# Kernel tuning notes

Hardware: AMD Instinct MI355X
Metric: run time of the kernel (lower is better)

The kernel has to match this reference:

```python
import jax, jax.numpy as jnp
import numpy as np

HEADS = 4


def _forward(x_atoms, pos, edge_attr, molecular_features, emb_W, emb_b, mp_W1, mp_b1, mp_W2, mp_b2, ln_g, ln_b, attn_in_w, attn_in_b, attn_out_w, attn_out_b, pool_W, pool_b, mol_gate, lrn_gate, molemb_W1, molemb_b1, molemb_W2, molemb_b2, lrnemb_W1, lrnemb_b1, lrnemb_W2, lrnemb_b2, fus_W1, fus_b1, fus_W2, fus_b2, head_W1, head_b1, head_W2, head_b2, edge_index, batch_idx):
    N = x_atoms.shape[0]
    B = molecular_features.shape[0]
    A = N // B  # equal-size molecules; batch_idx = repeat(arange(B), A)
    H = emb_W.shape[1]
    L = mp_W1.shape[0]
    src, dst = edge_index[0], edge_index[1]  # PyG: x_j = x[src], x_i = x[dst]
    x = x_atoms @ emb_W + emb_b
    # distance features (constant across layers)
    diff = pos[dst] - pos[src]
    d = jnp.sqrt(jnp.sum(diff * diff, axis=1, keepdims=True) + 1e-12)
    dist_feat = jnp.concatenate([d, 1.0 / (1.0 + d), jnp.exp(-d)], axis=1)  # [E,3]
    ones_e = jnp.ones((src.shape[0], 1), x.dtype)
    cnt = jnp.maximum(jax.ops.segment_sum(ones_e, dst, num_segments=N), 1.0)
    for l in range(L):
        res = x
        msg = jnp.concatenate([x[dst], x[src], dist_feat], axis=1)  # [E, 2H+3]
        msg = jax.nn.relu(msg @ mp_W1[l] + mp_b1[l]) @ mp_W2[l] + mp_b2[l]
        x = jax.ops.segment_sum(msg, dst, num_segments=N) / cnt  # mean aggregation
        y = x + res
        mu = y.mean(-1, keepdims=True)
        var = jnp.var(y, axis=-1, keepdims=True)
        x = (y - mu) * jax.lax.rsqrt(var + 1e-5) * ln_g[l] + ln_b[l]
    xm = x.reshape(B, A, H)
    explicit = xm.mean(axis=1)  # scatter_mean over equal-size graphs
    # per-molecule multi-head self-attention (torch MHA, eval mode)
    hd = H // HEADS
    qkv = xm @ attn_in_w.T + attn_in_b
    q, k, v = jnp.split(qkv, 3, axis=-1)
    q = q.reshape(B, A, HEADS, hd)
    k = k.reshape(B, A, HEADS, hd)
    v = v.reshape(B, A, HEADS, hd)
    scores = jnp.einsum('bqhd,bkhd->bhqk', q, k) / jnp.sqrt(jnp.asarray(hd, x.dtype))
    att = jax.nn.softmax(scores, axis=-1)
    o = jnp.einsum('bhqk,bkhd->bqhd', att, v).reshape(B, A, H)
    attended = o @ attn_out_w.T + attn_out_b
    aw = jax.nn.softmax(jnp.sum(attended * xm, axis=-1), axis=1)  # [B,A]
    wmean = jnp.sum(attended * aw[..., None], axis=1)
    maxp = attended.max(axis=1)
    meanp = attended.mean(axis=1)
    stdp = jnp.std(attended, axis=1, ddof=1)  # torch.std unbiased
    pooled = jnp.stack([wmean, maxp, meanp, stdp], axis=0)  # [4,B,H]
    proj = jnp.einsum('kbh,khf->kbf', pooled, pool_W) + pool_b[:, None, :]
    learned = jnp.moveaxis(proj, 0, 1).reshape(B, -1)  # [B,LF]
    # per-property gated MLPs, vectorized over P (atom gates are computed but unused in the source)
    gm = molecular_features[None] * jax.nn.sigmoid(mol_gate)[:, None, :]
    gl = learned[None] * jax.nn.sigmoid(lrn_gate)[:, None, :]
    molrep = jax.nn.relu(jnp.einsum('pbm,pmh->pbh', gm, molemb_W1) + molemb_b1[:, None, :])
    molrep = jnp.einsum('pbh,phk->pbk', molrep, molemb_W2) + molemb_b2[:, None, :]
    lrnrep = jax.nn.relu(jnp.einsum('pbm,pmh->pbh', gl, lrnemb_W1) + lrnemb_b1[:, None, :])
    lrnrep = jnp.einsum('pbh,phk->pbk', lrnrep, lrnemb_W2) + lrnemb_b2[:, None, :]
    P = mol_gate.shape[0]
    comb = jnp.concatenate([jnp.broadcast_to(explicit[None], (P, B, H)), molrep, lrnrep], axis=-1)
    fused = jax.nn.relu(jnp.einsum('pbc,pch->pbh', comb, fus_W1) + fus_b1[:, None, :])
    fused = jnp.einsum('pbh,phk->pbk', fused, fus_W2) + fus_b2[:, None, :]
    h = jax.nn.relu(jnp.einsum('pbh,phk->pbk', fused, head_W1) + head_b1[:, None, :])
    out = jnp.einsum('pbk,pko->pbo', h, head_W2) + head_b2[:, None, :]
    return out  # [P,B,1]: stacked predictions for the 4 properties


def setup_inputs() -> dict:
    key = jax.random.key(0)
    ks = jax.random.split(key, 24)
    B, A, F, M, H, LF, L, P = 1024, 32, 64, 200, 128, 64, 3, 4
    N = B * A
    E = N * 16
    H2, H4, Q = H // 2, H // 4, LF // 4
    n = lambda i, shape, s=1.0: jax.random.normal(ks[i], shape, dtype=jnp.float32) * s
    inp = {}
    inp['x_atoms'] = n(0, (N, F))
    inp['pos'] = n(1, (N, 3)) * 3.0
    inp['edge_attr'] = n(2, (E, 4))
    inp['molecular_features'] = n(3, (B, M))
    inp['emb_W'] = n(4, (F, H), 0.1)
    inp['emb_b'] = jnp.zeros((H,), jnp.float32)
    inp['mp_W1'] = n(5, (L, 2 * H + 3, H), 0.05)
    inp['mp_b1'] = jnp.zeros((L, H), jnp.float32)
    inp['mp_W2'] = n(6, (L, H, H), 0.05)
    inp['mp_b2'] = jnp.zeros((L, H), jnp.float32)
    inp['ln_g'] = jnp.ones((L, H), jnp.float32)
    inp['ln_b'] = jnp.zeros((L, H), jnp.float32)
    inp['attn_in_w'] = n(7, (3 * H, H), 0.08)
    inp['attn_in_b'] = jnp.zeros((3 * H,), jnp.float32)
    inp['attn_out_w'] = n(8, (H, H), 0.08)
    inp['attn_out_b'] = jnp.zeros((H,), jnp.float32)
    inp['pool_W'] = n(9, (4, H, Q), 0.08)
    inp['pool_b'] = jnp.zeros((4, Q), jnp.float32)
    inp['mol_gate'] = n(10, (P, M))
    inp['lrn_gate'] = n(11, (P, LF))
    inp['molemb_W1'] = n(12, (P, M, H2), 0.08)
    inp['molemb_b1'] = jnp.zeros((P, H2), jnp.float32)
    inp['molemb_W2'] = n(13, (P, H2, H2), 0.08)
    inp['molemb_b2'] = jnp.zeros((P, H2), jnp.float32)
    inp['lrnemb_W1'] = n(14, (P, LF, H2), 0.08)
    inp['lrnemb_b1'] = jnp.zeros((P, H2), jnp.float32)
    inp['lrnemb_W2'] = n(15, (P, H2, H2), 0.08)
    inp['lrnemb_b2'] = jnp.zeros((P, H2), jnp.float32)
    inp['fus_W1'] = n(16, (P, 2 * H, H), 0.08)
    inp['fus_b1'] = jnp.zeros((P, H), jnp.float32)
    inp['fus_W2'] = n(17, (P, H, H2), 0.08)
    inp['fus_b2'] = jnp.zeros((P, H2), jnp.float32)
    inp['head_W1'] = n(18, (P, H2, H4), 0.08)
    inp['head_b1'] = jnp.zeros((P, H4), jnp.float32)
    inp['head_W2'] = n(19, (P, H4, 1), 0.08)
    inp['head_b2'] = jnp.zeros((P, 1), jnp.float32)
    inp['edge_index'] = jax.random.randint(ks[20], (2, E), 0, N)
    inp['batch_idx'] = jnp.repeat(jnp.arange(B), A)
    return inp


def reference(x_atoms, pos, edge_attr, molecular_features, emb_W, emb_b, mp_W1, mp_b1, mp_W2, mp_b2, ln_g, ln_b, attn_in_w, attn_in_b, attn_out_w, attn_out_b, pool_W, pool_b, mol_gate, lrn_gate, molemb_W1, molemb_b1, molemb_W2, molemb_b2, lrnemb_W1, lrnemb_b1, lrnemb_W2, lrnemb_b2, fus_W1, fus_b1, fus_W2, fus_b2, head_W1, head_b1, head_W2, head_b2, edge_index, batch_idx):
    return _forward(x_atoms, pos, edge_attr, molecular_features, emb_W, emb_b, mp_W1, mp_b1, mp_W2, mp_b2, ln_g, ln_b, attn_in_w, attn_in_b, attn_out_w, attn_out_b, pool_W, pool_b, mol_gate, lrn_gate, molemb_W1, molemb_b1, molemb_W2, molemb_b2, lrnemb_W1, lrnemb_b1, lrnemb_W2, lrnemb_b2, fus_W1, fus_b1, fus_W2, fus_b2, head_W1, head_b1, head_W2, head_b2, edge_index, batch_idx)
```

## Files before the change

### kernel.cpp

```cpp
#include <hip/hip_runtime.h>

#define NE 524288
#define NN 32768
#define NB 1024

#define F4(p) (*(const float4*)(p))

typedef __bf16 bf16x8 __attribute__((ext_vector_type(8)));
typedef float  f32x4  __attribute__((ext_vector_type(4)));

__device__ __forceinline__ float sigmoidf_(float v) { return 1.f / (1.f + expf(-v)); }

__device__ __forceinline__ void bf16split(float f, short &hi, short &lo) {
  unsigned u = __float_as_uint(f);
  unsigned rh = (u + 0x7FFFu + ((u >> 16) & 1u)) >> 16;
  float fh = __uint_as_float(rh << 16);
  float fl = f - fh;
  unsigned u2 = __float_as_uint(fl);
  unsigned rl = (u2 + 0x7FFFu + ((u2 >> 16) & 1u)) >> 16;
  hi = (short)rh; lo = (short)rl;
}

__device__ __forceinline__ unsigned short f2bf(float f) {
  unsigned u = __float_as_uint(f);
// ... 19 lines not shown
    s = fmaf(xr[i],   ww.x, s);
    s = fmaf(xr[i+1], ww.y, s);
    s = fmaf(xr[i+2], ww.z, s);
    s = fmaf(xr[i+3], ww.w, s);
  }
  return s;
}

__global__ __launch_bounds__(128) void embed_kernel(
    const float* __restrict__ xa, const float* __restrict__ W,
    const float* __restrict__ b, float* __restrict__ x)
{
  __shared__ float a[64];
  const int n = blockIdx.x, t = threadIdx.x;
  if (t < 64) a[t] = xa[n*64 + t];
  __syncthreads();
  float s = b[t];
#pragma unroll 8
  for (int f = 0; f < 64; ++f) s = fmaf(a[f], W[f*128 + t], s);
  x[n*128 + t] = s;
}

__global__ __launch_bounds__(256) void hist_kernel(const int* __restrict__ ei, int* __restrict__ cnt) {
  const int e = blockIdx.x*256 + threadIdx.x;
  atomicAdd(&cnt[ei[NE + e]], 1);
}

__global__ __launch_bounds__(1024) void scan_kernel(
    const int* __restrict__ cnt, int* __restrict__ off, int* __restrict__ cur)
{
  __shared__ int wsum[16];
  const int t = threadIdx.x;
  int local[32];
  const int base = t*32;
  int s = 0;
#pragma unroll
  for (int i = 0; i < 32; ++i) { local[i] = cnt[base+i]; s += local[i]; }
  int pre = s;
  const int lane = t & 63;
#pragma unroll
  for (int o = 1; o < 64; o <<= 1) { int v = __shfl_up(pre, o); if (lane >= o) pre += v; }
  if (lane == 63) wsum[t >> 6] = pre;
  __syncthreads();
  if (t == 0) { int a = 0; for (int w = 0; w < 16; ++w) { int v = wsum[w]; wsum[w] = a; a += v; } }
  __syncthreads();
  int excl = wsum[t >> 6] + pre - s;
#pragma unroll
  for (int i = 0; i < 32; ++i) { off[base+i] = excl; cur[base+i] = excl; excl += local[i]; }
  if (t == 1023) off[NN] = excl;
}

__global__ __launch_bounds__(256) void scatter_kernel(
    const float* __restrict__ pos, const int* __restrict__ ei,
    int* __restrict__ cur, int* __restrict__ csr_src, float* __restrict__ csr_df)
{
  const int e = blockIdx.x*256 + threadIdx.x;
  const int s = ei[e];
  const int d = ei[NE + e];
  float dx = pos[d*3+0] - pos[s*3+0];
  float dy = pos[d*3+1] - pos[s*3+1];
  float dz = pos[d*3+2] - pos[s*3+2];
  float dist = sqrtf(dx*dx + dy*dy + dz*dz + 1e-12f);
  const int slot = atomicAdd(&cur[d], 1);
  csr_src[slot] = s;
  csr_df[slot*3+0] = dist;
  csr_df[slot*3+1] = 1.f/(1.f + dist);
  csr_df[slot*3+2] = expf(-dist);
}

__device__ __forceinline__ void pack_decode(int r, int N, int &k, int &n) {
  const int j = r & 7, lane = (r >> 3) & 63, rest = r >> 9;
  const int NT = N >> 4;
  const int t = rest % NT, kc = rest / NT;
  k = kc*32 + (lane >> 4)*8 + j;
  n = t*16 + (lane & 15);
}

__global__ __launch_bounds__(256) void prep_kernel(
    const float* __restrict__ mp_W1, const float* __restrict__ mp_W2,
    const float* __restrict__ win, const float* __restrict__ wout,
    const float* __restrict__ mp_b1,
    short* __restrict__ bh, short* __restrict__ bl, float* __restrict__ pqbias)
{
  const int i = blockIdx.x*256 + threadIdx.x;
  if (i < 768) { const int l = i >> 8, t = i & 255; pqbias[i] = t < 128 ? mp_b1[l*128 + t] : 0.f; }
  if (i >= 212992) return;
  int k, n; float v;
  if (i < 98304) {
    const int l = i / 32768, r = i % 32768;
    pack_decode(r, 256, k, n);
    const float* W = mp_W1 + (size_t)l*259*128;
    v = (n < 128) ? W[k*128 + n] : W[(128+k)*128 + (n-128)];
  } else if (i < 147456) {
    const int q = i - 98304, l = q / 16384, r = q % 16384;
    pack_decode(r, 128, k, n);
    v = mp_W2[(size_t)l*16384 + k*128 + n];
  } else if (i < 196608) {
    const int r = i - 147456;
    pack_decode(r, 384, k, n);
    v = win[n*128 + k];
  } else {
    const int r = i - 196608;
    pack_decode(r, 128, k, n);
    v = wout[n*128 + k];
  }
  short h, lo; bf16split(v, h, lo);
  bh[i] = h; bl[i] = lo;
}

__global__ __launch_bounds__(256, 2) void mfma_gemm_kernel(
    const float* __restrict__ A, int lda,
    const short* __restrict__ Bh, const short* __restrict__ Bl,
    const float* __restrict__ bias, float* __restrict__ C, int ncols, int ldc,
    unsigned short* __restrict__ qbf)
{
  const int lane = threadIdx.x & 63, wid = threadIdx.x >> 6;
  const int m0 = blockIdx.x * 128 + wid * 32;
  const int n0 = blockIdx.y * 64;
  const int NT = ncols >> 4;
  const int cl = lane & 15, kg = lane >> 4;

  bf16x8 Ah[2][4], Al[2][4];
#pragma unroll
  for (int s = 0; s < 2; ++s)
#pragma unroll
    for (int kc = 0; kc < 4; ++kc) {
      const float* ap = &A[(size_t)(m0 + s*16 + cl)*lda + kc*32 + kg*8];
      const float4 f0 = F4(ap), f1 = F4(ap + 4);
      const float fv[8] = {f0.x,f0.y,f0.z,f0.w,f1.x,f1.y,f1.z,f1.w};
      union { short s[8]; bf16x8 b; } uh, ul;
#pragma unroll
      for (int j = 0; j < 8; ++j) bf16split(fv[j], uh.s[j], ul.s[j]);
      Ah[s][kc] = uh.b; Al[s][kc] = ul.b;
    }

  f32x4 acc[2][4];
#pragma unroll
  for (int s = 0; s < 2; ++s)
#pragma unroll
    for (int t = 0; t < 4; ++t) acc[s][t] = (f32x4){0.f,0.f,0.f,0.f};

#pragma unroll
  for (int kc = 0; kc < 4; ++kc) {
    bf16x8 Bfh[4], Bfl[4];
#pragma unroll
    for (int t = 0; t < 4; ++t) {
      const size_t off = (((size_t)(kc*NT + (n0 >> 4) + t))*64 + lane)*8;
      Bfh[t] = *(const bf16x8*)&Bh[off];
      Bfl[t] = *(const bf16x8*)&Bl[off];
    }
#pragma unroll
    for (int s = 0; s < 2; ++s)
#pragma unroll
      for (int t = 0; t < 4; ++t)
        acc[s][t] = __builtin_amdgcn_mfma_f32_16x16x32_bf16(Ah[s][kc], Bfh[t], acc[s][t], 0, 0, 0);
#pragma unroll
    for (int s = 0; s < 2; ++s)
#pragma unroll
      for (int t = 0; t < 4; ++t)
        acc[s][t] = __builtin_amdgcn_mfma_f32_16x16x32_bf16(Ah[s][kc], Bfl[t], acc[s][t], 0, 0, 0);
#pragma unroll
    for (int s = 0; s < 2; ++s)
#pragma unroll
      for (int t = 0; t < 4; ++t)
        acc[s][t] = __builtin_amdgcn_mfma_f32_16x16x32_bf16(Al[s][kc], Bfh[t], acc[s][t], 0, 0, 0);
  }

#pragma unroll
  for (int t = 0; t < 4; ++t) {
    const int col = n0 + t*16 + cl;
    const float bv = bias[col];
#pragma unroll
    for (int s = 0; s < 2; ++s) {
      const int rbase = m0 + s*16 + kg*4;
#pragma unroll
      for (int r = 0; r < 4; ++r) {
        const float v = acc[s][t][r] + bv;
        if (qbf && col >= 128)
          qbf[(size_t)(rbase + r)*128 + (col - 128)] = f2bf(v);
        else
          C[(size_t)(rbase + r)*ldc + col] = v;
      }
    }
  }
}

__global__ __launch_bounds__(256, 2) void mfma_gemm_ln_kernel(
    const float* __restrict__ A, int lda,
    const short* __restrict__ Bh, const short* __restrict__ Bl,
    const float* __restrict__ b2, const int* __restrict__ csr_off,
    const float* __restrict__ g, const float* __restrict__ bb,
    float* __restrict__ x)
{
  const int lane = threadIdx.x & 63, wid = threadIdx.x >> 6;
  const int m0 = blockIdx.x * 64 + wid * 16;
  const int cl = lane & 15, kg = lane >> 4;

  bf16x8 Ah[4], Al[4];
#pragma unroll
  for (int kc = 0; kc < 4; ++kc) {
    const float* ap = &A[(size_t)(m0 + cl)*lda + kc*32 + kg*8];
    const float4 f0 = F4(ap), f1 = F4(ap + 4);
    const float fv[8] = {f0.x,f0.y,f0.z,f0.w,f1.x,f1.y,f1.z,f1.w};
    union { short s[8]; bf16x8 b; } uh, ul;
#pragma unroll
    for (int j = 0; j < 8; ++j) bf16split(fv[j], uh.s[j], ul.s[j]);
    Ah[kc] = uh.b; Al[kc] = ul.b;
  }

  f32x4 acc[8];
#pragma unroll
  for (int t = 0; t < 8; ++t) acc[t] = (f32x4){0.f,0.f,0.f,0.f};

#pragma unroll
  for (int kc = 0; kc < 4; ++kc) {
    bf16x8 Bfh[8], Bfl[8];
#pragma unroll
    for (int t = 0; t < 8; ++t) {
      const size_t off = (((size_t)(kc*8 + t))*64 + lane)*8;
      Bfh[t] = *(const bf16x8*)&Bh[off];
      Bfl[t] = *(const bf16x8*)&Bl[off];
    }
#pragma unroll
    for (int t = 0; t < 8; ++t)
      acc[t] = __builtin_amdgcn_mfma_f32_16x16x32_bf16(Ah[kc], Bfh[t], acc[t], 0, 0, 0);
#pragma unroll
    for (int t = 0; t < 8; ++t)
      acc[t] = __builtin_amdgcn_mfma_f32_16x16x32_bf16(Ah[kc], Bfl[t], acc[t], 0, 0, 0);
#pragma unroll
    for (int t = 0; t < 8; ++t)
      acc[t] = __builtin_amdgcn_mfma_f32_16x16x32_bf16(Al[kc], Bfh[t], acc[t], 0, 0, 0);
  }

  const int r0 = m0 + kg*4;
  float sflag[4];
#pragma unroll
  for (int r = 0; r < 4; ++r)
    sflag[r] = (csr_off[r0 + r + 1] > csr_off[r0 + r]) ? 1.f : 0.f;

  float ps[4] = {0.f,0.f,0.f,0.f}, pq[4] = {0.f,0.f,0.f,0.f};
  float yv[8][4];
#pragma unroll
  for (int t = 0; t < 8; ++t) {
    const int col = t*16 + cl;
    const float b2v = b2[col];
#pragma unroll
    for (int r = 0; r < 4; ++r) {
      const float y = acc[t][r] + sflag[r]*b2v + x[(size_t)(r0 + r)*128 + col];
      yv[t][r] = y;
      ps[r] += y;
      pq[r] = fmaf(y, y, pq[r]);
    }
  }
#pragma unroll
  for (int o = 1; o < 16; o <<= 1) {
#pragma unroll
    for (int r = 0; r < 4; ++r) { ps[r] += __shfl_xor(ps[r], o); pq[r] += __shfl_xor(pq[r], o); }
  }
#pragma unroll
  for (int r = 0; r < 4; ++r) {
    const float mu = ps[r] * (1.f/128.f);
    const float var = pq[r]*(1.f/128.f) - mu*mu;
    const float rstd = rsqrtf(var + 1e-5f);
#pragma unroll
    for (int t = 0; t < 8; ++t) {
      const int col = t*16 + cl;
      x[(size_t)(r0 + r)*128 + col] = (yv[t][r] - mu)*rstd*g[col] + bb[col];
    }
  }
}

__global__ __launch_bounds__(256, 6) void agg_kernel(
    float* __restrict__ P, const unsigned short* __restrict__ Qbf,
    const int* __restrict__ csr_off, const int* __restrict__ csr_src,
    const float* __restrict__ csr_df, const float* __restrict__ W1)
{
  const int tid = threadIdx.x;
  const int node = blockIdx.x*4 + (tid >> 6);
  const int lane = tid & 63;
  const int c0 = lane*2;
  const int off0 = csr_off[node], off1 = csr_off[node+1];

  const float* __restrict__ w1c = W1 + 256*128;
  const float w00 = w1c[c0],       w01 = w1c[c0+1];
  const float w10 = w1c[128+c0],   w11 = w1c[128+c0+1];
  const float w20 = w1c[256+c0],   w21 = w1c[256+c0+1];
  const float2 p = *(const float2*)&P[(size_t)node*128 + c0];

  float a0 = 0.f, a1 = 0.f;
  int e = off0;
  for (; e + 8 <= off1; e += 8) {
    int sr[8];
#pragma unroll
    for (int j = 0; j < 8; ++j) sr[j] = csr_src[e+j];
    ushort2 qv[8];
#pragma unroll
    for (int j = 0; j < 8; ++j) qv[j] = *(const ushort2*)&Qbf[(size_t)sr[j]*128 + c0];
    float dfv[8][3];
#pragma unroll
    for (int j = 0; j < 8; ++j) {
      dfv[j][0] = csr_df[(e+j)*3+0];
      dfv[j][1] = csr_df[(e+j)*3+1];
      dfv[j][2] = csr_df[(e+j)*3+2];
    }
#pragma unroll
    for (int j = 0; j < 8; ++j) {
      float h0 = p.x + bf2f(qv[j].x);
      h0 = fmaf(dfv[j][0], w00, h0); h0 = fmaf(dfv[j][1], w10, h0); h0 = fmaf(dfv[j][2], w20, h0);
      float h1 = p.y + bf2f(qv[j].y);
      h1 = fmaf(dfv[j][0], w01, h1); h1 = fmaf(dfv[j][1], w11, h1); h1 = fmaf(dfv[j][2], w21, h1);
      a0 += fmaxf(h0, 0.f);
      a1 += fmaxf(h1, 0.f);
    }
  }
  for (; e < off1; ++e) {
    const ushort2 qv = *(const ushort2*)&Qbf[(size_t)csr_src[e]*128 + c0];
    const float d0 = csr_df[e*3+0], d1 = csr_df[e*3+1], d2 = csr_df[e*3+2];
    float h0 = p.x + bf2f(qv.x);
    h0 = fmaf(d0, w00, h0); h0 = fmaf(d1, w10, h0); h0 = fmaf(d2, w20, h0);
    float h1 = p.y + bf2f(qv.y);
    h1 = fmaf(d0, w01, h1); h1 = fmaf(d1, w11, h1); h1 = fmaf(d2, w21, h1);
    a0 += fmaxf(h0, 0.f);
    a1 += fmaxf(h1, 0.f);
  }
  const int deg = off1 - off0;
  const float rc = deg > 0 ? 1.f/(float)deg : 1.f;
  *(float2*)&P[(size_t)node*128 + c0] = make_float2(a0*rc, a1*rc);
}

__global__ __launch_bounds__(128) void attn_kernel(float* __restrict__ dqkv)
{
  __shared__ float sk[32*132];
  __shared__ float sv[32*132];
  const int tid = threadIdx.x;
  const int b = blockIdx.x;

  for (int idx = tid; idx < 1024; idx += 128) {
    const int a = idx >> 5, c4 = idx & 31;
    *(float4*)&sk[a*132 + c4*4] = F4(&dqkv[(size_t)(b*32+a)*384 + 128 + c4*4]);
    *(float4*)&sv[a*132 + c4*4] = F4(&dqkv[(size_t)(b*32+a)*384 + 256 + c4*4]);
  }
  __syncthreads();

  const int h = tid >> 5, qr = tid & 31;
  float qreg[32];
  ld32(qreg, &dqkv[(size_t)(b*32+qr)*384 + h*32]);

  float sc[32];
#pragma unroll
  for (int k = 0; k < 32; ++k)
    sc[k] = dot32r(&sk[k*132 + h*32], qreg) * 0.17677669529663687f;
  float mx = sc[0];
#pragma unroll
  for (int k = 1; k < 32; ++k) mx = fmaxf(mx, sc[k]);
  float se = 0.f;
#pragma unroll
  for (int k = 0; k < 32; ++k) { sc[k] = expf(sc[k] - mx); se += sc[k]; }
  const float inv = 1.f / se;

  __syncthreads();

  float od[32];
#pragma unroll
  for (int i = 0; i < 32; ++i) od[i] = 0.f;
#pragma unroll 4
  for (int k = 0; k < 32; ++k) {
    const float w = sc[k] * inv;
    const float* vr = &sv[k*132 + h*32];
#pragma unroll
    for (int i = 0; i < 32; i += 4) {
      float4 v = F4(&vr[i]);
      od[i]   = fmaf(w, v.x, od[i]);
      od[i+1] = fmaf(w, v.y, od[i+1]);
      od[i+2] = fmaf(w, v.z, od[i+2]);
      od[i+3] = fmaf(w, v.w, od[i+3]);
    }
  }
#pragma unroll
  for (int i = 0; i < 32; i += 4)
    *(float4*)&sk[qr*132 + h*32 + i] = make_float4(od[i], od[i+1], od[i+2], od[i+3]);
  __syncthreads();

  for (int idx = tid; idx < 1024; idx += 128) {
    const int a = idx >> 5, c4 = idx & 31;
    *(float4*)&dqkv[(size_t)(b*32+a)*384 + 256 + c4*4] = F4(&sk[a*132 + c4*4]);
  }
}

__global__ __launch_bounds__(128) void pool_kernel(
    const float* __restrict__ att, const float* __restrict__ x,
    const float* __restrict__ pW, const float* __restrict__ pb,
    float* __restrict__ expl, float* __restrict__ lrn)
{
  __shared__ float satt[32*132];
  __shared__ float sx[32*132];
  __shared__ float aw_l[32];
  __shared__ float spool[512];
  const int tid = threadIdx.x;
  const int b = blockIdx.x;

  for (int idx = tid; idx < 1024; idx += 128) {
    const int a = idx >> 5, c4 = idx & 31;
    *(float4*)&satt[a*132 + c4*4] = F4(&att[(size_t)(b*32+a)*128 + c4*4]);
    *(float4*)&sx[a*132 + c4*4]   = F4(&x[(size_t)(b*32+a)*128 + c4*4]);
  }
  __syncthreads();

  {
    const int a = tid >> 2, q4 = tid & 3;
    float sp = 0.f;
#pragma unroll
    for (int i = 0; i < 32; ++i)
      sp = fmaf(satt[a*132 + q4*32 + i], sx[a*132 + q4*32 + i], sp);
    sp += __shfl_xor(sp, 1);
    sp += __shfl_xor(sp, 2);
    if (q4 == 0) aw_l[a] = sp;
  }
  __syncthreads();

  {
    float awr[32];
    float mxl = aw_l[0];
#pragma unroll
    for (int a = 1; a < 32; ++a) mxl = fmaxf(mxl, aw_l[a]);
    float se = 0.f;
#pragma unroll
    for (int a = 0; a < 32; ++a) { awr[a] = expf(aw_l[a] - mxl); se += awr[a]; }
    const float inv = 1.f / se;
    const int c = tid;
    float mx = -3.4e38f, sm = 0.f, wm = 0.f, ex = 0.f;
#pragma unroll
    for (int a = 0; a < 32; ++a) {
      const float v = satt[a*132 + c];
      mx = fmaxf(mx, v);
      sm += v;
      wm = fmaf(v, awr[a], wm);
      ex += sx[a*132 + c];
    }
    wm *= inv;
    const float mean = sm * 0.03125f;
    float s2 = 0.f;
#pragma unroll
    for (int a = 0; a < 32; ++a) {
      const float d = satt[a*132 + c] - mean;
      s2 = fmaf(d, d, s2);
    }
    const float stdp = sqrtf(s2 * (1.f/31.f));
    expl[b*128 + c] = ex * 0.03125f;
    spool[c]       = wm;
    spool[128 + c] = mx;
    spool[256 + c] = mean;
    spool[384 + c] = stdp;
  }
  __syncthreads();

  if (tid < 64) {
    const int k = tid >> 4, qq = tid & 15;
    const float* pk = pW + k*2048;
    float s0 = 0.f, s1 = 0.f, s2 = 0.f, s3 = 0.f;
    for (int h2 = 0; h2 < 128; h2 += 4) {
      s0 = fmaf(spool[k*128 + h2],   pk[h2*16 + qq],     s0);
      s1 = fmaf(spool[k*128 + h2+1], pk[(h2+1)*16 + qq], s1);
      s2 = fmaf(spool[k*128 + h2+2], pk[(h2+2)*16 + qq], s2);
      s3 = fmaf(spool[k*128 + h2+3], pk[(h2+3)*16 + qq], s3);
    }
    lrn[b*64 + tid] = pb[k*16 + qq] + (s0+s1) + (s2+s3);
  }
}

__global__ __launch_bounds__(64) void head_kernel(
    const float* __restrict__ molf, const float* __restrict__ lrn,
    const float* __restrict__ expl,
    const float* __restrict__ mol_gate, const float* __restrict__ lrn_gate,
    const float* __restrict__ meW1, const float* __restrict__ meb1,
    const float* __restrict__ meW2, const float* __restrict__ meb2,
    const float* __restrict__ leW1, const float* __restrict__ leb1,
    const float* __restrict__ leW2, const float* __restrict__ leb2,
    const float* __restrict__ fW1, const float* __restrict__ fb1,
    const float* __restrict__ fW2, const float* __restrict__ fb2,
    const float* __restrict__ hW1, const float* __restrict__ hb1,
    const float* __restrict__ hW2, const float* __restrict__ hb2,
    float* __restrict__ out)
{
  const int b = blockIdx.x, p = blockIdx.y, t = threadIdx.x;
  __shared__ float sgm[200];
  __shared__ float sgl[64];
  __shared__ float sA[64];
  __shared__ float sB[64];
  __shared__ float scomb[256];
  __shared__ float sf1[128];
  __shared__ float sf2[64];

  for (int m = t; m < 200; m += 64)
    sgm[m] = molf[b*200 + m] * sigmoidf_(mol_gate[p*200 + m]);
  sgl[t] = lrn[b*64 + t] * sigmoidf_(lrn_gate[p*64 + t]);
  scomb[t]      = expl[b*128 + t];
  scomb[64 + t] = expl[b*128 + 64 + t];
  __syncthreads();

  {
    const float* w = meW1 + p*12800;
    float a0=0.f,a1=0.f,a2=0.f,a3=0.f;
    for (int m = 0; m < 200; m += 4) {
      a0 = fmaf(sgm[m],   w[m*64 + t],       a0);
      a1 = fmaf(sgm[m+1], w[(m+1)*64 + t],   a1);
      a2 = fmaf(sgm[m+2], w[(m+2)*64 + t],   a2);
      a3 = fmaf(sgm[m+3], w[(m+3)*64 + t],   a3);
    }
    sA[t] = fmaxf(meb1[p*64 + t] + (a0+a1) + (a2+a3), 0.f);
    const float* w2 = leW1 + p*4096;
    float b0=0.f,b1_=0.f,b2_=0.f,b3=0.f;
    for (int m = 0; m < 64; m += 4) {
      b0  = fmaf(sgl[m],   w2[m*64 + t],     b0);
      b1_ = fmaf(sgl[m+1], w2[(m+1)*64 + t], b1_);
      b2_ = fmaf(sgl[m+2], w2[(m+2)*64 + t], b2_);
      b3  = fmaf(sgl[m+3], w2[(m+3)*64 + t], b3);
    }
    sB[t] = fmaxf(leb1[p*64 + t] + (b0+b1_) + (b2_+b3), 0.f);
  }
  __syncthreads();
  {
    const float* w = meW2 + p*4096;
    float a0=0.f,a1=0.f,a2=0.f,a3=0.f;
    for (int h = 0; h < 64; h += 4) {
      a0 = fmaf(sA[h],   w[h*64 + t],       a0);
      a1 = fmaf(sA[h+1], w[(h+1)*64 + t],   a1);
      a2 = fmaf(sA[h+2], w[(h+2)*64 + t],   a2);
      a3 = fmaf(sA[h+3], w[(h+3)*64 + t],   a3);
    }
    scomb[128 + t] = meb2[p*64 + t] + (a0+a1) + (a2+a3);
    const float* w2 = leW2 + p*4096;
    float b0=0.f,b1_=0.f,b2_=0.f,b3=0.f;
    for (int h = 0; h < 64; h += 4) {
      b0  = fmaf(sB[h],   w2[h*64 + t],     b0);
      b1_ = fmaf(sB[h+1], w2[(h+1)*64 + t], b1_);
      b2_ = fmaf(sB[h+2], w2[(h+2)*64 + t], b2_);
      b3  = fmaf(sB[h+3], w2[(h+3)*64 + t], b3);
    }
    scomb[192 + t] = leb2[p*64 + t] + (b0+b1_) + (b2_+b3);
  }
  __syncthreads();
  {
    const float* w = fW1 + p*32768;
    float s00=0.f,s01=0.f,s02=0.f,s03=0.f;
    float s10=0.f,s11=0.f,s12=0.f,s13=0.f;
    for (int c = 0; c < 256; c += 4) {
      const float v0 = scomb[c], v1 = scomb[c+1], v2 = scomb[c+2], v3 = scomb[c+3];
      s00 = fmaf(v0, w[c*128 + t],          s00);
      s01 = fmaf(v1, w[(c+1)*128 + t],      s01);
      s02 = fmaf(v2, w[(c+2)*128 + t],      s02);
      s03 = fmaf(v3, w[(c+3)*128 + t],      s03);
      s10 = fmaf(v0, w[c*128 + 64 + t],     s10);
      s11 = fmaf(v1, w[(c+1)*128 + 64 + t], s11);
      s12 = fmaf(v2, w[(c+2)*128 + 64 + t], s12);
      s13 = fmaf(v3, w[(c+3)*128 + 64 + t], s13);
    }
    sf1[t]      = fmaxf(fb1[p*128 + t]      + (s00+s01) + (s02+s03), 0.f);
    sf1[64 + t] = fmaxf(fb1[p*128 + 64 + t] + (s10+s11) + (s12+s13), 0.f);
  }
  __syncthreads();
  {
    const float* w = fW2 + p*8192;
    float a0=0.f,a1=0.f,a2=0.f,a3=0.f;
    for (int h = 0; h < 128; h += 4) {
      a0 = fmaf(sf1[h],   w[h*64 + t],       a0);
      a1 = fmaf(sf1[h+1], w[(h+1)*64 + t],   a1);
      a2 = fmaf(sf1[h+2], w[(h+2)*64 + t],   a2);
      a3 = fmaf(sf1[h+3], w[(h+3)*64 + t],   a3);
    }
    sf2[t] = fb2[p*64 + t] + (a0+a1) + (a2+a3);
  }
  __syncthreads();
  float val = 0.f;
  if (t < 32) {
    const float* w = hW1 + p*2048;
    float a0=0.f,a1=0.f,a2=0.f,a3=0.f;
    for (int h = 0; h < 64; h += 4) {
      a0 = fmaf(sf2[h],   w[h*32 + t],       a0);
      a1 = fmaf(sf2[h+1], w[(h+1)*32 + t],   a1);
      a2 = fmaf(sf2[h+2], w[(h+2)*32 + t],   a2);
      a3 = fmaf(sf2[h+3], w[(h+3)*32 + t],   a3);
    }
    val = fmaxf(hb1[p*32 + t] + (a0+a1) + (a2+a3), 0.f) * hW2[p*32 + t];
  }
#pragma unroll
  for (int o = 1; o < 32; o <<= 1) val += __shfl_xor(val, o);
  if (t == 0) out[p*1024 + b] = val + hb2[p];
}

extern "C" void kernel_launch(void* const* d_in, const int* in_sizes, int n_in,
                              void* d_out, int out_size, void* d_ws, size_t ws_size,
                              hipStream_t stream) {
  const float* x_atoms    = (const float*)d_in[0];
  const float* pos        = (const float*)d_in[1];
  const float* molf       = (const float*)d_in[3];
  const float* emb_W      = (const float*)d_in[4];
  const float* emb_b      = (const float*)d_in[5];
  const float* mp_W1      = (const float*)d_in[6];
  const float* mp_b1      = (const float*)d_in[7];
  const float* mp_W2      = (const float*)d_in[8];
  const float* mp_b2      = (const float*)d_in[9];
  const float* ln_g       = (const float*)d_in[10];
  const float* ln_b       = (const float*)d_in[11];
  const float* attn_in_w  = (const float*)d_in[12];
  const float* attn_in_b  = (const float*)d_in[13];
  const float* attn_out_w = (const float*)d_in[14];
  const float* attn_out_b = (const float*)d_in[15];
  const float* pool_W     = (const float*)d_in[16];
  const float* pool_b     = (const float*)d_in[17];
  const float* mol_gate   = (const float*)d_in[18];
  const float* lrn_gate   = (const float*)d_in[19];
  const float* meW1       = (const float*)d_in[20];
  const float* meb1       = (const float*)d_in[21];
  const float* meW2       = (const float*)d_in[22];
  const float* meb2       = (const float*)d_in[23];
  const float* leW1       = (const float*)d_in[24];
  const float* leb1       = (const float*)d_in[25];
  const float* leW2       = (const float*)d_in[26];
  const float* leb2       = (const float*)d_in[27];
  const float* fW1        = (const float*)d_in[28];
  const float* fb1        = (const float*)d_in[29];
  const float* fW2        = (const float*)d_in[30];
  const float* fb2        = (const float*)d_in[31];
  const float* hW1        = (const float*)d_in[32];
  const float* hb1        = (const float*)d_in[33];
  const float* hW2        = (const float*)d_in[34];
  const float* hb2        = (const float*)d_in[35];
  const int*   ei         = (const int*)d_in[36];

  float* ws      = (float*)d_ws;
  float* x       = ws;
  float* region  = x + (size_t)NN*128;
  float* P       = region;
  unsigned short* Qbf = (unsigned short*)(region + (size_t)NN*128);
  float* dqkv    = region;
  float* att     = region + (size_t)NN*384;
  float* csr_df  = att + (size_t)NN*128;
  int*   csr_src = (int*)(csr_df + (size_t)NE*3);
  int*   cnt_i   = csr_src + NE;
  int*   csr_off = cnt_i + NN;
  int*   cur     = csr_off + NN + 1;
  float* lrn     = (float*)(cur + NN);
  float* expl    = lrn + NB*64;
  float* pqbias  = expl + NB*128;
  short* bh      = (short*)(pqbias + 768);
  short* bl      = bh + 212992;

  const int W1AB_OFF = 0;
  const int W2_OFF   = 98304;
  const int WIN_OFF  = 147456;
  const int WOUT_OFF = 196608;

  hipMemsetAsync(cnt_i, 0, (size_t)NN*sizeof(int), stream);

  embed_kernel<<<NN, 128, 0, stream>>>(x_atoms, emb_W, emb_b, x);
  hist_kernel<<<NE/256, 256, 0, stream>>>(ei, cnt_i);
  scan_kernel<<<1, 1024, 0, stream>>>(cnt_i, csr_off, cur);
  scatter_kernel<<<NE/256, 256, 0, stream>>>(pos, ei, cur, csr_src, csr_df);
  prep_kernel<<<(212992 + 255)/256, 256, 0, stream>>>(mp_W1, mp_W2, attn_in_w, attn_out_w,
                                                      mp_b1, bh, bl, pqbias);

  for (int l = 0; l < 3; ++l) {
    mfma_gemm_kernel<<<dim3(NN/128, 4), 256, 0, stream>>>(
        x, 128, bh + W1AB_OFF + l*32768, bl + W1AB_OFF + l*32768,
        pqbias + l*256, P, 256, 128, Qbf);
    agg_kernel<<<NN/4, 256, 0, stream>>>(P, Qbf, csr_off, csr_src, csr_df,
                                         mp_W1 + (size_t)l*259*128);
    mfma_gemm_ln_kernel<<<NN/64, 256, 0, stream>>>(
        P, 128, bh + W2_OFF + l*16384, bl + W2_OFF + l*16384,
        mp_b2 + l*128, csr_off, ln_g + l*128, ln_b + l*128, x);
  }

  mfma_gemm_kernel<<<dim3(NN/128, 6), 256, 0, stream>>>(
      x, 128, bh + WIN_OFF, bl + WIN_OFF, attn_in_b, dqkv, 384, 384, nullptr);
  attn_kernel<<<NB, 128, 0, stream>>>(dqkv);
  mfma_gemm_kernel<<<dim3(NN/128, 2), 256, 0, stream>>>(
      dqkv + 256, 384, bh + WOUT_OFF, bl + WOUT_OFF, attn_out_b, att, 128, 128, nullptr);
  pool_kernel<<<NB, 128, 0, stream>>>(att, x, pool_W, pool_b, expl, lrn);
  head_kernel<<<dim3(NB, 4), 64, 0, stream>>>(molf, lrn, expl, mol_gate, lrn_gate,
      meW1, meb1, meW2, meb2, leW1, leb1, leW2, leb2,
      fW1, fb1, fW2, fb2, hW1, hb1, hW2, hb2, (float*)d_out);
}
```

Baseline: 429.0 us.

## Run head MLPs as block-diagonal MFMA GEMMs and pack CSR edge records

Replaces the scalar per-molecule head kernel with a chain of split-bf16 MFMA GEMMs. The four parallel heads become block-diagonal packed weights, with the gates folded into the first-layer weights during prep. The edge CSR is also repacked into a single float4 record per edge (source index plus three distance features) so the aggregation loop needs one vector load instead of four. The GEMM kernel gains a runtime K loop, ReLU and strided output columns. The cost is extra launches, redundant work on the zero blocks of the block-diagonal weights, and a larger weight-prep kernel.

```diff
diff --git a/kernel.cpp b/kernel.cpp
--- a/kernel.cpp
+++ b/kernel.cpp
@@ -95,7 +95,7 @@
 
 __global__ __launch_bounds__(256) void scatter_kernel(
     const float* __restrict__ pos, const int* __restrict__ ei,
-    int* __restrict__ cur, int* __restrict__ csr_src, float* __restrict__ csr_df)
+    int* __restrict__ cur, float4* __restrict__ csr_rec)
 {
   const int e = blockIdx.x*256 + threadIdx.x;
   const int s = ei[e];
@@ -105,10 +105,7 @@
   float dz = pos[d*3+2] - pos[s*3+2];
   float dist = sqrtf(dx*dx + dy*dy + dz*dz + 1e-12f);
   const int slot = atomicAdd(&cur[d], 1);
-  csr_src[slot] = s;
-  csr_df[slot*3+0] = dist;
-  csr_df[slot*3+1] = 1.f/(1.f + dist);
-  csr_df[slot*3+2] = expf(-dist);
+  csr_rec[slot] = make_float4(__int_as_float(s), dist, 1.f/(1.f + dist), expf(-dist));
 }
 
 __device__ __forceinline__ void pack_decode(int r, int N, int &k, int &n) {
@@ -119,42 +116,87 @@
   n = t*16 + (lane & 15);
 }
 
+#define W1AB_OFF 0
+#define W2_OFF   98304
+#define WIN_OFF  147456
+#define WOUT_OFF 196608
+#define HA_OFF   212992
+#define HB_OFF   270336
+#define HL_OFF   335872
+#define HD_OFF   352256
+#define HF1_OFF  417792
+#define HF2_OFF  942080
+#define HH1_OFF  1073152
+#define PK_TOTAL 1105920
+
 __global__ __launch_bounds__(256) void prep_kernel(
     const float* __restrict__ mp_W1, const float* __restrict__ mp_W2,
     const float* __restrict__ win, const float* __restrict__ wout,
     const float* __restrict__ mp_b1,
+    const float* __restrict__ mol_gate, const float* __restrict__ lrn_gate,
+    const float* __restrict__ meW1, const float* __restrict__ meW2,
+    const float* __restrict__ leW1, const float* __restrict__ leW2,
+    const float* __restrict__ fW1, const float* __restrict__ fW2,
+    const float* __restrict__ hW1,
     short* __restrict__ bh, short* __restrict__ bl, float* __restrict__ pqbias)
 {
   const int i = blockIdx.x*256 + threadIdx.x;
   if (i < 768) { const int l = i >> 8, t = i & 255; pqbias[i] = t < 128 ? mp_b1[l*128 + t] : 0.f; }
-  if (i >= 212992) return;
+  if (i >= PK_TOTAL) return;
   int k, n; float v;
-  if (i < 98304) {
+  if (i < W2_OFF) {
     const int l = i / 32768, r = i % 32768;
     pack_decode(r, 256, k, n);
     const float* W = mp_W1 + (size_t)l*259*128;
     v = (n < 128) ? W[k*128 + n] : W[(128+k)*128 + (n-128)];
-  } else if (i < 147456) {
-    const int q = i - 98304, l = q / 16384, r = q % 16384;
+  } else if (i < WIN_OFF) {
+    const int q = i - W2_OFF, l = q / 16384, r = q % 16384;
     pack_decode(r, 128, k, n);
     v = mp_W2[(size_t)l*16384 + k*128 + n];
-  } else if (i < 196608) {
-    const int r = i - 147456;
-    pack_decode(r, 384, k, n);
+  } else if (i < WOUT_OFF) {
+    pack_decode(i - WIN_OFF, 384, k, n);
     v = win[n*128 + k];
+  } else if (i < HA_OFF) {
+    pack_decode(i - WOUT_OFF, 128, k, n);
+    v = wout[n*128 + k];
+  } else if (i < HB_OFF) {
+    pack_decode(i - HA_OFF, 256, k, n);
+    const int p = n >> 6, h = n & 63;
+    v = (k < 200) ? meW1[p*12800 + k*64 + h] * sigmoidf_(mol_gate[p*200 + k]) : 0.f;
+  } else if (i < HL_OFF) {
+    pack_decode(i - HB_OFF, 256, k, n);
+    const int p = n >> 6, h = n & 63, kp = k >> 6, c = k & 63;
+    v = (kp == p) ? meW2[p*4096 + c*64 + h] : 0.f;
+  } else if (i < HD_OFF) {
+    pack_decode(i - HL_OFF, 256, k, n);
+    const int p = n >> 6, h = n & 63;
+    v = leW1[p*4096 + k*64 + h] * sigmoidf_(lrn_gate[p*64 + k]);
+  } else if (i < HF1_OFF) {
+    pack_decode(i - HD_OFF, 256, k, n);
+    const int p = n >> 6, h = n & 63, kp = k >> 6, c = k & 63;
+    v = (kp == p) ? leW2[p*4096 + c*64 + h] : 0.f;
+  } else if (i < HF2_OFF) {
+    pack_decode(i - HF1_OFF, 512, k, n);
+    const int p = n >> 7, h = n & 127, kp = k >> 8, c = k & 255;
+    v = (kp == p) ? fW1[p*32768 + c*128 + h] : 0.f;
+  } else if (i < HH1_OFF) {
+    pack_decode(i - HF2_OFF, 256, k, n);
+    const int p = n >> 6, h = n & 63, kp = k >> 7, c = k & 127;
+    v = (kp == p) ? fW2[p*8192 + c*64 + h] : 0.f;
   } else {
-    const int r = i - 196608;
-    pack_decode(r, 128, k, n);
-    v = wout[n*128 + k];
-  }
-  short h, lo; bf16split(v, h, lo);
-  bh[i] = h; bl[i] = lo;
+    pack_decode(i - HH1_OFF, 128, k, n);
+    const int p = n >> 5, h = n & 31, kp = k >> 6, c = k & 63;
+    v = (kp == p) ? hW1[p*2048 + c*32 + h] : 0.f;
+  }
+  short h_, lo; bf16split(v, h_, lo);
+  bh[i] = h_; bl[i] = lo;
 }
 
 __global__ __launch_bounds__(256, 2) void mfma_gemm_kernel(
-    const float* __restrict__ A, int lda,
+    const float* __restrict__ A, int lda, int K,
     const short* __restrict__ Bh, const short* __restrict__ Bl,
     const float* __restrict__ bias, float* __restrict__ C, int ncols, int ldc,
+    int colstride, int coloff, int relu,
     unsigned short* __restrict__ qbf)
 {
   const int lane = threadIdx.x & 63, wid = threadIdx.x >> 6;
@@ -162,29 +204,26 @@
   const int n0 = blockIdx.y * 64;
   const int NT = ncols >> 4;
   const int cl = lane & 15, kg = lane >> 4;
-
-  bf16x8 Ah[2][4], Al[2][4];
+  const int KC = K >> 5;
+
+  f32x4 acc[2][4];
 #pragma unroll
   for (int s = 0; s < 2; ++s)
 #pragma unroll
-    for (int kc = 0; kc < 4; ++kc) {
+    for (int t = 0; t < 4; ++t) acc[s][t] = (f32x4){0.f,0.f,0.f,0.f};
+
+  for (int kc = 0; kc < KC; ++kc) {
+    bf16x8 Ah[2], Al[2];
+#pragma unroll
+    for (int s = 0; s < 2; ++s) {
       const float* ap = &A[(size_t)(m0 + s*16 + cl)*lda + kc*32 + kg*8];
       const float4 f0 = F4(ap), f1 = F4(ap + 4);
       const float fv[8] = {f0.x,f0.y,f0.z,f0.w,f1.x,f1.y,f1.z,f1.w};
       union { short s[8]; bf16x8 b; } uh, ul;
 #pragma unroll
       for (int j = 0; j < 8; ++j) bf16split(fv[j], uh.s[j], ul.s[j]);
-      Ah[s][kc] = uh.b; Al[s][kc] = ul.b;
-    }
-
-  f32x4 acc[2][4];
-#pragma unroll
-  for (int s = 0; s < 2; ++s)
-#pragma unroll
-    for (int t = 0; t < 4; ++t) acc[s][t] = (f32x4){0.f,0.f,0.f,0.f};
-
-#pragma unroll
-  for (int kc = 0; kc < 4; ++kc) {
+      Ah[s] = uh.b; Al[s] = ul.b;
+    }
     bf16x8 Bfh[4], Bfl[4];
 #pragma unroll
     for (int t = 0; t < 4; ++t) {
@@ -196,33 +235,35 @@
     for (int s = 0; s < 2; ++s)
 #pragma unroll
       for (int t = 0; t < 4; ++t)
-        acc[s][t] = __builtin_amdgcn_mfma_f32_16x16x32_bf16(Ah[s][kc], Bfh[t], acc[s][t], 0, 0, 0);
+        acc[s][t] = __builtin_amdgcn_mfma_f32_16x16x32_bf16(Ah[s], Bfh[t], acc[s][t], 0, 0, 0);
 #pragma unroll
     for (int s = 0; s < 2; ++s)
 #pragma unroll
       for (int t = 0; t < 4; ++t)
-        acc[s][t] = __builtin_amdgcn_mfma_f32_16x16x32_bf16(Ah[s][kc], Bfl[t], acc[s][t], 0, 0, 0);
+        acc[s][t] = __builtin_amdgcn_mfma_f32_16x16x32_bf16(Ah[s], Bfl[t], acc[s][t], 0, 0, 0);
 #pragma unroll
     for (int s = 0; s < 2; ++s)
 #pragma unroll
       for (int t = 0; t < 4; ++t)
-        acc[s][t] = __builtin_amdgcn_mfma_f32_16x16x32_bf16(Al[s][kc], Bfh[t], acc[s][t], 0, 0, 0);
+        acc[s][t] = __builtin_amdgcn_mfma_f32_16x16x32_bf16(Al[s], Bfh[t], acc[s][t], 0, 0, 0);
   }
 
 #pragma unroll
   for (int t = 0; t < 4; ++t) {
     const int col = n0 + t*16 + cl;
     const float bv = bias[col];
+    const int dstcol = (col >> 6)*colstride + coloff + (col & 63);
 #pragma unroll
     for (int s = 0; s < 2; ++s) {
       const int rbase = m0 + s*16 + kg*4;
 #pragma unroll
       for (int r = 0; r < 4; ++r) {
-        const float v = acc[s][t][r] + bv;
+        float v = acc[s][t][r] + bv;
+        if (relu) v = fmaxf(v, 0.f);
         if (qbf && col >= 128)
           qbf[(size_t)(rbase + r)*128 + (col - 128)] = f2bf(v);
         else
-          C[(size_t)(rbase + r)*ldc + col] = v;
+          C[(size_t)(rbase + r)*ldc + dstcol] = v;
       }
     }
   }
@@ -315,8 +356,8 @@
 
 __global__ __launch_bounds__(256, 6) void agg_kernel(
     float* __restrict__ P, const unsigned short* __restrict__ Qbf,
-    const int* __restrict__ csr_off, const int* __restrict__ csr_src,
-    const float* __restrict__ csr_df, const float* __restrict__ W1)
+    const int* __restrict__ csr_off, const float4* __restrict__ csr_rec,
+    const float* __restrict__ W1)
 {
   const int tid = threadIdx.x;
   const int node = blockIdx.x*4 + (tid >> 6);
@@ -333,42 +374,36 @@
   float a0 = 0.f, a1 = 0.f;
   int e = off0;
   for (; e + 8 <= off1; e += 8) {
-    int sr[8];
-#pragma unroll
-    for (int j = 0; j < 8; ++j) sr[j] = csr_src[e+j];
+    float4 rc[8];
+#pragma unroll
+    for (int j = 0; j < 8; ++j) rc[j] = csr_rec[e+j];
     ushort2 qv[8];
 #pragma unroll
-    for (int j = 0; j < 8; ++j) qv[j] = *(const ushort2*)&Qbf[(size_t)sr[j]*128 + c0];
-    float dfv[8][3];
-#pragma unroll
-    for (int j = 0; j < 8; ++j) {
-      dfv[j][0] = csr_df[(e+j)*3+0];
-      dfv[j][1] = csr_df[(e+j)*3+1];
-      dfv[j][2] = csr_df[(e+j)*3+2];
-    }
+    for (int j = 0; j < 8; ++j)
+      qv[j] = *(const ushort2*)&Qbf[(size_t)__float_as_int(rc[j].x)*128 + c0];
 #pragma unroll
     for (int j = 0; j < 8; ++j) {
       float h0 = p.x + bf2f(qv[j].x);
-      h0 = fmaf(dfv[j][0], w00, h0); h0 = fmaf(dfv[j][1], w10, h0); h0 = fmaf(dfv[j][2], w20, h0);
+      h0 = fmaf(rc[j].y, w00, h0); h0 = fmaf(rc[j].z, w10, h0); h0 = fmaf(rc[j].w, w20, h0);
       float h1 = p.y + bf2f(qv[j].y);
-      h1 = fmaf(dfv[j][0], w01, h1); h1 = fmaf(dfv[j][1], w11, h1); h1 = fmaf(dfv[j][2], w21, h1);
+      h1 = fmaf(rc[j].y, w01, h1); h1 = fmaf(rc[j].z, w11, h1); h1 = fmaf(rc[j].w, w21, h1);
       a0 += fmaxf(h0, 0.f);
       a1 += fmaxf(h1, 0.f);
     }
   }
   for (; e < off1; ++e) {
-    const ushort2 qv = *(const ushort2*)&Qbf[(size_t)csr_src[e]*128 + c0];
-    const float d0 = csr_df[e*3+0], d1 = csr_df[e*3+1], d2 = csr_df[e*3+2];
+    const float4 rc = csr_rec[e];
+    const ushort2 qv = *(const ushort2*)&Qbf[(size_t)__float_as_int(rc.x)*128 + c0];
     float h0 = p.x + bf2f(qv.x);
-    h0 = fmaf(d0, w00, h0); h0 = fmaf(d1, w10, h0); h0 = fmaf(d2, w20, h0);
+    h0 = fmaf(rc.y, w00, h0); h0 = fmaf(rc.z, w10, h0); h0 = fmaf(rc.w, w20, h0);
     float h1 = p.y + bf2f(qv.y);
-    h1 = fmaf(d0, w01, h1); h1 = fmaf(d1, w11, h1); h1 = fmaf(d2, w21, h1);
+    h1 = fmaf(rc.y, w01, h1); h1 = fmaf(rc.z, w11, h1); h1 = fmaf(rc.w, w21, h1);
     a0 += fmaxf(h0, 0.f);
     a1 += fmaxf(h1, 0.f);
   }
   const int deg = off1 - off0;
-  const float rc = deg > 0 ? 1.f/(float)deg : 1.f;
-  *(float2*)&P[(size_t)node*128 + c0] = make_float2(a0*rc, a1*rc);
+  const float rc_ = deg > 0 ? 1.f/(float)deg : 1.f;
+  *(float2*)&P[(size_t)node*128 + c0] = make_float2(a0*rc_, a1*rc_);
 }
 
 __global__ __launch_bounds__(128) void attn_kernel(float* __restrict__ dqkv)
@@ -433,7 +468,7 @@
 __global__ __launch_bounds__(128) void pool_kernel(
     const float* __restrict__ att, const float* __restrict__ x,
     const float* __restrict__ pW, const float* __restrict__ pb,
-    float* __restrict__ expl, float* __restrict__ lrn)
+    float* __restrict__ expl, float* __restrict__ lrn, float* __restrict__ comb)
 {
   __shared__ float satt[32*132];
   __shared__ float sx[32*132];
@@ -489,7 +524,11 @@
       s2 = fmaf(d, d, s2);
     }
     const float stdp = sqrtf(s2 * (1.f/31.f));
-    expl[b*128 + c] = ex * 0.03125f;
+    const float exm = ex * 0.03125f;
+    expl[b*128 + c] = exm;
+#pragma unroll
+    for (int p = 0; p < 4; ++p)
+      comb[(size_t)b*1024 + p*256 + c] = exm;
     spool[c]       = wm;
     spool[128 + c] = mx;
     spool[256 + c] = mean;
@@ -511,124 +550,30 @@
   }
 }
 
-__global__ __launch_bounds__(64) void head_kernel(
-    const float* __restrict__ molf, const float* __restrict__ lrn,
-    const float* __restrict__ expl,
-    const float* __restrict__ mol_gate, const float* __restrict__ lrn_gate,
-    const float* __restrict__ meW1, const float* __restrict__ meb1,
-    const float* __restrict__ meW2, const float* __restrict__ meb2,
-    const float* __restrict__ leW1, const float* __restrict__ leb1,
-    const float* __restrict__ leW2, const float* __restrict__ leb2,
-    const float* __restrict__ fW1, const float* __restrict__ fb1,
-    const float* __restrict__ fW2, const float* __restrict__ fb2,
-    const float* __restrict__ hW1, const float* __restrict__ hb1,
-    const float* __restrict__ hW2, const float* __restrict__ hb2,
-    float* __restrict__ out)
-{
-  const int b = blockIdx.x, p = blockIdx.y, t = threadIdx.x;
-  __shared__ float sgm[200];
-  __shared__ float sgl[64];
-  __shared__ float sA[64];
-  __shared__ float sB[64];
-  __shared__ float scomb[256];
-  __shared__ float sf1[128];
-  __shared__ float sf2[64];
-
-  for (int m = t; m < 200; m += 64)
-    sgm[m] = molf[b*200 + m] * sigmoidf_(mol_gate[p*200 + m]);
-  sgl[t] = lrn[b*64 + t] * sigmoidf_(lrn_gate[p*64 + t]);
-  scomb[t]      = expl[b*128 + t];
-  scomb[64 + t] = expl[b*128 + 64 + t];
-  __syncthreads();
-
-  {
-    const float* w = meW1 + p*12800;
-    float a0=0.f,a1=0.f,a2=0.f,a3=0.f;
-    for (int m = 0; m < 200; m += 4) {
-      a0 = fmaf(sgm[m],   w[m*64 + t],       a0);
-      a1 = fmaf(sgm[m+1], w[(m+1)*64 + t],   a1);
-      a2 = fmaf(sgm[m+2], w[(m+2)*64 + t],   a2);
-      a3 = fmaf(sgm[m+3], w[(m+3)*64 + t],   a3);
-    }
-    sA[t] = fmaxf(meb1[p*64 + t] + (a0+a1) + (a2+a3), 0.f);
-    const float* w2 = leW1 + p*4096;
-    float b0=0.f,b1_=0.f,b2_=0.f,b3=0.f;
-    for (int m = 0; m < 64; m += 4) {
-      b0  = fmaf(sgl[m],   w2[m*64 + t],     b0);
-      b1_ = fmaf(sgl[m+1], w2[(m+1)*64 + t], b1_);
-      b2_ = fmaf(sgl[m+2], w2[(m+2)*64 + t], b2_);
-      b3  = fmaf(sgl[m+3], w2[(m+3)*64 + t], b3);
-    }
-    sB[t] = fmaxf(leb1[p*64 + t] + (b0+b1_) + (b2_+b3), 0.f);
-  }
-  __syncthreads();
-  {
-    const float* w = meW2 + p*4096;
-    float a0=0.f,a1=0.f,a2=0.f,a3=0.f;
-    for (int h = 0; h < 64; h += 4) {
-      a0 = fmaf(sA[h],   w[h*64 + t],       a0);
-      a1 = fmaf(sA[h+1], w[(h+1)*64 + t],   a1);
-      a2 = fmaf(sA[h+2], w[(h+2)*64 + t],   a2);
-      a3 = fmaf(sA[h+3], w[(h+3)*64 + t],   a3);
-    }
-    scomb[128 + t] = meb2[p*64 + t] + (a0+a1) + (a2+a3);
-    const float* w2 = leW2 + p*4096;
-    float b0=0.f,b1_=0.f,b2_=0.f,b3=0.f;
-    for (int h = 0; h < 64; h += 4) {
-      b0  = fmaf(sB[h],   w2[h*64 + t],     b0);
-      b1_ = fmaf(sB[h+1], w2[(h+1)*64 + t], b1_);
-      b2_ = fmaf(sB[h+2], w2[(h+2)*64 + t], b2_);
-      b3  = fmaf(sB[h+3], w2[(h+3)*64 + t], b3);
-    }
-    scomb[192 + t] = leb2[p*64 + t] + (b0+b1_) + (b2_+b3);
-  }
-  __syncthreads();
-  {
-    const float* w = fW1 + p*32768;
-    float s00=0.f,s01=0.f,s02=0.f,s03=0.f;
-    float s10=0.f,s11=0.f,s12=0.f,s13=0.f;
-    for (int c = 0; c < 256; c += 4) {
-      const float v0 = scomb[c], v1 = scomb[c+1], v2 = scomb[c+2], v3 = scomb[c+3];
-      s00 = fmaf(v0, w[c*128 + t],          s00);
-      s01 = fmaf(v1, w[(c+1)*128 + t],      s01);
-      s02 = fmaf(v2, w[(c+2)*128 + t],      s02);
-      s03 = fmaf(v3, w[(c+3)*128 + t],      s03);
-      s10 = fmaf(v0, w[c*128 + 64 + t],     s10);
-      s11 = fmaf(v1, w[(c+1)*128 + 64 + t], s11);
-      s12 = fmaf(v2, w[(c+2)*128 + 64 + t], s12);
-      s13 = fmaf(v3, w[(c+3)*128 + 64 + t], s13);
-    }
-    sf1[t]      = fmaxf(fb1[p*128 + t]      + (s00+s01) + (s02+s03), 0.f);
-    sf1[64 + t] = fmaxf(fb1[p*128 + 64 + t] + (s10+s11) + (s12+s13), 0.f);
-  }
-  __syncthreads();
-  {
-    const float* w = fW2 + p*8192;
-    float a0=0.f,a1=0.f,a2=0.f,a3=0.f;
-    for (int h = 0; h < 128; h += 4) {
-      a0 = fmaf(sf1[h],   w[h*64 + t],       a0);
-      a1 = fmaf(sf1[h+1], w[(h+1)*64 + t],   a1);
-      a2 = fmaf(sf1[h+2], w[(h+2)*64 + t],   a2);
-      a3 = fmaf(sf1[h+3], w[(h+3)*64 + t],   a3);
-    }
-    sf2[t] = fb2[p*64 + t] + (a0+a1) + (a2+a3);
-  }
-  __syncthreads();
-  float val = 0.f;
-  if (t < 32) {
-    const float* w = hW1 + p*2048;
-    float a0=0.f,a1=0.f,a2=0.f,a3=0.f;
-    for (int h = 0; h < 64; h += 4) {
-      a0 = fmaf(sf2[h],   w[h*32 + t],       a0);
-      a1 = fmaf(sf2[h+1], w[(h+1)*32 + t],   a1);
-      a2 = fmaf(sf2[h+2], w[(h+2)*32 + t],   a2);
-      a3 = fmaf(sf2[h+3], w[(h+3)*32 + t],   a3);
-    }
-    val = fmaxf(hb1[p*32 + t] + (a0+a1) + (a2+a3), 0.f) * hW2[p*32 + t];
-  }
-#pragma unroll
-  for (int o = 1; o < 32; o <<= 1) val += __shfl_xor(val, o);
-  if (t == 0) out[p*1024 + b] = val + hb2[p];
+__global__ __launch_bounds__(256) void padmolf_kernel(
+    const float* __restrict__ molf, float* __restrict__ mp)
+{
+  const int i = blockIdx.x*256 + threadIdx.x;
+  const int b = i / 224, m = i - b*224;
+  mp[i] = (m < 200) ? molf[b*200 + m] : 0.f;
+}
+
+__global__ __launch_bounds__(256) void outdot_kernel(
+    const float* __restrict__ H1, const float* __restrict__ hW2,
+    const float* __restrict__ hb2, float* __restrict__ out)
+{
+  const int id = blockIdx.x*256 + threadIdx.x;
+  const int b = id & 1023, p = id >> 10;
+  const float* hp = &H1[(size_t)b*128 + p*32];
+  const float* wp = &hW2[p*32];
+  float s0=0.f,s1=0.f,s2=0.f,s3=0.f;
+  for (int h = 0; h < 32; h += 4) {
+    s0 = fmaf(hp[h],   wp[h],   s0);
+    s1 = fmaf(hp[h+1], wp[h+1], s1);
+    s2 = fmaf(hp[h+2], wp[h+2], s2);
+    s3 = fmaf(hp[h+3], wp[h+3], s3);
+  }
+  out[p*1024 + b] = (s0+s1) + (s2+s3) + hb2[p];
 }
 
 extern "C" void kernel_launch(void* const* d_in, const int* in_sizes, int n_in,
@@ -678,36 +623,41 @@
   unsigned short* Qbf = (unsigned short*)(region + (size_t)NN*128);
   float* dqkv    = region;
   float* att     = region + (size_t)NN*384;
-  float* csr_df  = att + (size_t)NN*128;
-  int*   csr_src = (int*)(csr_df + (size_t)NE*3);
-  int*   cnt_i   = csr_src + NE;
+  float* csr_rf  = att + (size_t)NN*128;
+  float4* csr_rec = (float4*)csr_rf;
+  int*   cnt_i   = (int*)(csr_rf + (size_t)NE*4);
   int*   csr_off = cnt_i + NN;
-  int*   cur     = csr_off + NN + 1;
+  int*   cur     = csr_off + NN + 64;
   float* lrn     = (float*)(cur + NN);
   float* expl    = lrn + NB*64;
   float* pqbias  = expl + NB*128;
   short* bh      = (short*)(pqbias + 768);
-  short* bl      = bh + 212992;
-
-  const int W1AB_OFF = 0;
-  const int W2_OFF   = 98304;
-  const int WIN_OFF  = 147456;
-  const int WOUT_OFF = 196608;
+  short* bl      = bh + PK_TOTAL;
+
+  float* molfPad = region;
+  float* MOLR1   = region + 229376;
+  float* LRNR1   = region + 491520;
+  float* COMB    = region + 753664;
+  float* FUS1    = region + 1802240;
+  float* FUS2    = region + 2326528;
+  float* H1      = region + 2588672;
 
   hipMemsetAsync(cnt_i, 0, (size_t)NN*sizeof(int), stream);
 
   embed_kernel<<<NN, 128, 0, stream>>>(x_atoms, emb_W, emb_b, x);
   hist_kernel<<<NE/256, 256, 0, stream>>>(ei, cnt_i);
   scan_kernel<<<1, 1024, 0, stream>>>(cnt_i, csr_off, cur);
-  scatter_kernel<<<NE/256, 256, 0, stream>>>(pos, ei, cur, csr_src, csr_df);
-  prep_kernel<<<(212992 + 255)/256, 256, 0, stream>>>(mp_W1, mp_W2, attn_in_w, attn_out_w,
-                                                      mp_b1, bh, bl, pqbias);
+  scatter_kernel<<<NE/256, 256, 0, stream>>>(pos, ei, cur, csr_rec);
+  prep_kernel<<<(PK_TOTAL + 255)/256, 256, 0, stream>>>(
+      mp_W1, mp_W2, attn_in_w, attn_out_w, mp_b1,
+      mol_gate, lrn_gate, meW1, meW2, leW1, leW2, fW1, fW2, hW1,
+      bh, bl, pqbias);
 
   for (int l = 0; l < 3; ++l) {
     mfma_gemm_kernel<<<dim3(NN/128, 4), 256, 0, stream>>>(
-        x, 128, bh + W1AB_OFF + l*32768, bl + W1AB_OFF + l*32768,
-        pqbias + l*256, P, 256, 128, Qbf);
-    agg_kernel<<<NN/4, 256, 0, stream>>>(P, Qbf, csr_off, csr_src, csr_df,
+        x, 128, 128, bh + W1AB_OFF + l*32768, bl + W1AB_OFF + l*32768,
+        pqbias + l*256, P, 256, 128, 64, 0, 0, Qbf);
+    agg_kernel<<<NN/4, 256, 0, stream>>>(P, Qbf, csr_off, csr_rec,
                                          mp_W1 + (size_t)l*259*128);
     mfma_gemm_ln_kernel<<<NN/64, 256, 0, stream>>>(
         P, 128, bh + W2_OFF + l*16384, bl + W2_OFF + l*16384,
@@ -715,12 +665,26 @@
   }
 
   mfma_gemm_kernel<<<dim3(NN/128, 6), 256, 0, stream>>>(
-      x, 128, bh + WIN_OFF, bl + WIN_OFF, attn_in_b, dqkv, 384, 384, nullptr);
+      x, 128, 128, bh + WIN_OFF, bl + WIN_OFF, attn_in_b, dqkv, 384, 384, 64, 0, 0, nullptr);
   attn_kernel<<<NB, 128, 0, stream>>>(dqkv);
   mfma_gemm_kernel<<<dim3(NN/128, 2), 256, 0, stream>>>(
-      dqkv + 256, 384, bh + WOUT_OFF, bl + WOUT_OFF, attn_out_b, att, 128, 128, nullptr);
-  pool_kernel<<<NB, 128, 0, stream>>>(att, x, pool_W, pool_b, expl, lrn);
-  head_kernel<<<dim3(NB, 4), 64, 0, stream>>>(molf, lrn, expl, mol_gate, lrn_gate,
-      meW1, meb1, meW2, meb2, leW1, leb1, leW2, leb2,
-      fW1, fb1, fW2, fb2, hW1, hb1, hW2, hb2, (float*)d_out);
-}
+      dqkv + 256, 384, 128, bh + WOUT_OFF, bl + WOUT_OFF, attn_out_b, att, 128, 128, 64, 0, 0, nullptr);
+  pool_kernel<<<NB, 128, 0, stream>>>(att, x, pool_W, pool_b, expl, lrn, COMB);
+
+  padmolf_kernel<<<(1024*224)/256, 256, 0, stream>>>(molf, molfPad);
+  mfma_gemm_kernel<<<dim3(8, 4), 256, 0, stream>>>(
+      molfPad, 224, 224, bh + HA_OFF, bl + HA_OFF, meb1, MOLR1, 256, 256, 64, 0, 1, nullptr);
+  mfma_gemm_kernel<<<dim3(8, 4), 256, 0, stream>>>(
+      MOLR1, 256, 256, bh + HB_OFF, bl + HB_OFF, meb2, COMB, 256, 1024, 256, 128, 0, nullptr);
+  mfma_gemm_kernel<<<dim3(8, 4), 256, 0, stream>>>(
+      lrn, 64, 64, bh + HL_OFF, bl + HL_OFF, leb1, LRNR1, 256, 256, 64, 0, 1, nullptr);
+  mfma_gemm_kernel<<<dim3(8, 4), 256, 0, stream>>>(
+      LRNR1, 256, 256, bh + HD_OFF, bl + HD_OFF, leb2, COMB, 256, 1024, 256, 192, 0, nullptr);
+  mfma_gemm_kernel<<<dim3(8, 8), 256, 0, stream>>>(
+      COMB, 1024, 1024, bh + HF1_OFF, bl + HF1_OFF, fb1, FUS1, 512, 512, 64, 0, 1, nullptr);
+  mfma_gemm_kernel<<<dim3(8, 4), 256, 0, stream>>>(
+      FUS1, 512, 512, bh + HF2_OFF, bl + HF2_OFF, fb2, FUS2, 256, 256, 64, 0, 0, nullptr);
+  mfma_gemm_kernel<<<dim3(8, 2), 256, 0, stream>>>(
+      FUS2, 256, 256, bh + HH1_OFF, bl + HH1_OFF, hb1, H1, 128, 128, 64, 0, 1, nullptr);
+  outdot_kernel<<<16, 256, 0, stream>>>(H1, hW2, hb2, (float*)d_out);
+}
```

Result: slower. 472.5 us (+10.1%).
